# Optimization experiments

Measured on AMD Instinct MI355X. Metric: run time of the kernel, lower is better.

Reference implementation:

```python
import jax, jax.numpy as jnp
import numpy as np

N_NODES = 100000
N_EDGES = 500000
IN_FEATS = 128
HID = 128
OUT = 1


def setup_inputs() -> dict:
    key = jax.random.key(0)
    ks = jax.random.split(key, 10)
    h = jax.random.normal(ks[0], (N_NODES, IN_FEATS), dtype=jnp.float32)
    src = jax.random.randint(ks[1], (N_EDGES,), 0, N_NODES, dtype=jnp.int32)
    dst = jax.random.randint(ks[2], (N_EDGES,), 0, N_NODES, dtype=jnp.int32)
    # Linear params (PyTorch convention: W [out,in], y = x @ W.T + b)
    s1 = 1.0 / np.sqrt(2 * IN_FEATS)
    s2 = 1.0 / np.sqrt(HID)
    W1 = jax.random.uniform(ks[3], (HID, 2 * IN_FEATS), jnp.float32, -s1, s1)
    b1 = jax.random.uniform(ks[4], (HID,), jnp.float32, -s1, s1)
    W2 = jax.random.uniform(ks[5], (HID, HID), jnp.float32, -s2, s2)
    b2 = jax.random.uniform(ks[6], (HID,), jnp.float32, -s2, s2)
    W3 = jax.random.uniform(ks[7], (OUT, HID), jnp.float32, -s2, s2)
    b3 = jax.random.uniform(ks[8], (OUT,), jnp.float32, -s2, s2)
    return {"h": h, "src": src, "dst": dst,
            "W1": W1, "b1": b1, "W2": W2, "b2": b2, "W3": W3, "b3": b3}


def reference(h, src, dst, W1, b1, W2, b2, W3, b3):
    # Per-edge gather of src/dst node features. Instead of materializing the
    # [E, 2*in] concat, split W1 into its src/dst halves and fuse the concat
    # into two GEMMs (same math as fc1(cat([h_u, h_v], 1))).
    h_u = h[src]                                   # [E, in]
    h_v = h[dst]                                   # [E, in]
    W1u, W1v = W1[:, :IN_FEATS], W1[:, IN_FEATS:]  # [hid, in] each
    x = h_u @ W1u.T + h_v @ W1v.T + b1             # [E, hid]
    x = jax.nn.relu(x)
    x = jax.nn.relu(x @ W2.T + b2)                 # [E, hid]
    score = x @ W3.T + b3                          # [E, out]
    return score
```

## Files before the change

kernel.cpp:

```cpp
#include <hip/hip_runtime.h>
#include <hip/hip_bf16.h>
#include <hip/hip_fp16.h>


#define N_NODES 100000
#define N_EDGES 500000
#define F       128
#define HID     128
#define TE      64
#define NT      ((N_EDGES + TE - 1) / TE)
#define GRID    512
#define BLOCK   512

typedef _Float16 f16x8 __attribute__((ext_vector_type(8)));
typedef float    f32x4 __attribute__((ext_vector_type(4)));

typedef __attribute__((address_space(3))) unsigned int  lds_u32;
typedef __attribute__((address_space(1))) const unsigned int glb_u32;

__device__ __forceinline__ void load_lds16(const void* g, void* l) {
    __builtin_amdgcn_global_load_lds((glb_u32*)g, (lds_u32*)l, 16, 0, 0);
}

__device__ __forceinline__ void bar_lgkm() {
    asm volatile("s_waitcnt lgkmcnt(0)" ::: "memory");
    __builtin_amdgcn_s_barrier();
    __builtin_amdgcn_sched_barrier(0);
}
__device__ __forceinline__ void bar_vm() {
    asm volatile("s_waitcnt vmcnt(0) lgkmcnt(0)" ::: "memory");
    __builtin_amdgcn_s_barrier();
    __builtin_amdgcn_sched_barrier(0);
}

__global__ __launch_bounds__(256) void h_to_f16(const float* __restrict__ h,
                                                _Float16* __restrict__ h16) {
    const int i = (blockIdx.x * 256 + threadIdx.x) * 8;
    float4 a = *(const float4*)(h + i);
    float4 b = *(const float4*)(h + i + 4);
    f16x8 v;
    v[0] = (_Float16)a.x; v[1] = (_Float16)a.y; v[2] = (_Float16)a.z; v[3] = (_Float16)a.w;
    v[4] = (_Float16)b.x; v[5] = (_Float16)b.y; v[6] = (_Float16)b.z; v[7] = (_Float16)b.w;
    *(f16x8*)(h16 + i) = v;
}

__global__ __launch_bounds__(BLOCK) void edge_mlp_v2(
    const _Float16* __restrict__ h16,
    const int*   __restrict__ src,
    const int*   __restrict__ dst,
    const float* __restrict__ W1,
    const float* __restrict__ b1,
    const float* __restrict__ W2,
    const float* __restrict__ b2,
    const float* __restrict__ W3,
    const float* __restrict__ b3,
    float*       __restrict__ out)
{
    __shared__ __align__(128) char Alds[2 * TE * 512];
    __shared__ __align__(128) char Xlds[TE * 256];

    const int tid  = threadIdx.x;
    const int wave = tid >> 6;
    const int lane = tid & 63;
    const int l15  = lane & 15;
    const int lk   = lane >> 4;

    const int n1 = wave * 16 + l15;

    f16x8 w1f[8];
    #pragma unroll
    for (int kt = 0; kt < 8; ++kt) {
        const float* p = W1 + n1 * 256 + kt * 32 + lk * 8;
        f16x8 v;
        #pragma unroll
        for (int j = 0; j < 8; ++j) v[j] = (_Float16)p[j];
        w1f[kt] = v;
    }
    const float b1v = b1[n1];

    f16x8 w2f[4];
    #pragma unroll
    for (int kt = 0; kt < 4; ++kt) {
        const float* p = W2 + n1 * 128 + kt * 32 + lk * 8;
        f16x8 v;
        #pragma unroll
        for (int j = 0; j < 8; ++j) v[j] = (_Float16)p[j];
        w2f[kt] = v;
    }
    const float b2v = b2[n1];

    float w3r[16];
    {
        const float* p = W3 + (tid & 7) * 16;
        #pragma unroll
        for (int i = 0; i < 16; ++i) w3r[i] = p[i];
    }
    const float b3v = b3[0];

    int eloc[4], k16v[4];
    #pragma unroll
    for (int j = 0; j < 4; ++j) {
        const int i = wave * 4 + j;
        eloc[j] = 2 * i + (lane >> 5);
        k16v[j] = (l15) ^ (eloc[j] & 7);
    }
    const int whichv = (lane >> 4) & 1;
    const int* idxp  = whichv ? dst : src;

    const int t0 = blockIdx.x;

    int nodeCur[4], nodeNext[4];

    #pragma unroll
    for (int j = 0; j < 4; ++j) {
        int eg = t0 * TE + eloc[j];
        if (eg >= N_EDGES) eg = N_EDGES - 1;
        nodeCur[j] = idxp[eg];
    }
    #pragma unroll
    for (int j = 0; j < 4; ++j) {
        const _Float16* g = h16 + (size_t)nodeCur[j] * F + k16v[j] * 8;
        load_lds16(g, Alds + (wave * 4 + j) * 1024);
    }
    {
        int tn = t0 + GRID; if (tn > NT - 1) tn = NT - 1;
        #pragma unroll
        for (int j = 0; j < 4; ++j) {
            int eg = tn * TE + eloc[j];
            if (eg >= N_EDGES) eg = N_EDGES - 1;
            nodeNext[j] = idxp[eg];
        }
    }

    int cur = 0;
    for (int t = t0; t < NT; t += GRID) {
        bar_vm();

        #pragma unroll
        for (int j = 0; j < 4; ++j) nodeCur[j] = nodeNext[j];
        {
            char* nb = Alds + (cur ^ 1) * (TE * 512);
            #pragma unroll
            for (int j = 0; j < 4; ++j) {
                const _Float16* g = h16 + (size_t)nodeCur[j] * F + k16v[j] * 8;
                load_lds16(g, nb + (wave * 4 + j) * 1024);
            }
        }
        {
            int tn2 = t + 2 * GRID; if (tn2 > NT - 1) tn2 = NT - 1;
            #pragma unroll
            for (int j = 0; j < 4; ++j) {
                int eg = tn2 * TE + eloc[j];
                if (eg >= N_EDGES) eg = N_EDGES - 1;
                nodeNext[j] = idxp[eg];
            }
        }

        const char* Ab = Alds + cur * (TE * 512);

        #pragma unroll
        for (int m = 0; m < 4; ++m) {
            f32x4 acc = {0.f, 0.f, 0.f, 0.f};
            #pragma unroll
            for (int kt = 0; kt < 8; ++kt) {
                const int edge = m * 16 + l15;
                int byte = edge * 512 + (kt * 32 + lk * 8) * 2;
                byte ^= (edge & 7) << 4;
                f16x8 a = *(const f16x8*)(Ab + byte);
                acc = __builtin_amdgcn_mfma_f32_16x16x32_f16(a, w1f[kt], acc, 0, 0, 0);
            }
            #pragma unroll
            for (int r = 0; r < 4; ++r) {
                float v = acc[r] + b1v;
                v = v > 0.f ? v : 0.f;
                const int edge = m * 16 + lk * 4 + r;
                int byte = edge * 256 + n1 * 2;
                byte ^= (edge & 7) << 4;
                *(_Float16*)(Xlds + byte) = (_Float16)v;
            }
        }
        bar_lgkm();

        f32x4 acc2[4];
        #pragma unroll
        for (int m = 0; m < 4; ++m) {
            f32x4 acc = {0.f, 0.f, 0.f, 0.f};
            #pragma unroll
            for (int kt = 0; kt < 4; ++kt) {
                const int edge = m * 16 + l15;
                int byte = edge * 256 + (kt * 32 + lk * 8) * 2;
                byte ^= (edge & 7) << 4;
                f16x8 a = *(const f16x8*)(Xlds + byte);
                acc = __builtin_amdgcn_mfma_f32_16x16x32_f16(a, w2f[kt], acc, 0, 0, 0);
            }
            acc2[m] = acc;
        }
        bar_lgkm();
        #pragma unroll
        for (int m = 0; m < 4; ++m) {
            #pragma unroll
            for (int r = 0; r < 4; ++r) {
                float v = acc2[m][r] + b2v;
                v = v > 0.f ? v : 0.f;
                const int edge = m * 16 + lk * 4 + r;
                int byte = edge * 256 + n1 * 2;
                byte ^= (edge & 7) << 4;
                *(_Float16*)(Xlds + byte) = (_Float16)v;
            }
        }
        bar_lgkm();

        {
            const int e_loc = tid >> 3;
            const int cgrp  = tid & 7;
            const int swz   = (e_loc & 7) << 4;
            const int base  = e_loc * 256 + cgrp * 32;
            f16x8 x0 = *(const f16x8*)(Xlds + (base ^ swz));
            f16x8 x1 = *(const f16x8*)(Xlds + ((base + 16) ^ swz));
            float p = 0.f;
            #pragma unroll
            for (int i = 0; i < 8; ++i) p += (float)x0[i] * w3r[i];
            #pragma unroll
            for (int i = 0; i < 8; ++i) p += (float)x1[i] * w3r[8 + i];
            p += __shfl_xor(p, 1);
            p += __shfl_xor(p, 2);
            p += __shfl_xor(p, 4);
            const int eg = t * TE + e_loc;
            if (cgrp == 0 && eg < N_EDGES) out[eg] = p + b3v;
        }
        cur ^= 1;
    }
}

__global__ __launch_bounds__(BLOCK) void edge_mlp_v1(
    const float* __restrict__ h,
    const int*   __restrict__ src,
    const int*   __restrict__ dst,
    const float* __restrict__ W1,
    const float* __restrict__ b1,
    const float* __restrict__ W2,
    const float* __restrict__ b2,
    const float* __restrict__ W3,
    const float* __restrict__ b3,
    float*       __restrict__ out)
{
    __shared__ __align__(128) char Alds[TE * 512];
    __shared__ __align__(128) char Xlds[TE * 256];

    const int tid  = threadIdx.x;
    const int wave = tid >> 6;
    const int lane = tid & 63;
    const int l15  = lane & 15;
    const int lk   = lane >> 4;

    const int n1 = wave * 16 + l15;

    f16x8 w1f[8];
    #pragma unroll
    for (int kt = 0; kt < 8; ++kt) {
        const float* p = W1 + n1 * 256 + kt * 32 + lk * 8;
        f16x8 v;
        #pragma unroll
        for (int j = 0; j < 8; ++j) v[j] = (_Float16)p[j];
        w1f[kt] = v;
    }
    const float b1v = b1[n1];

    f16x8 w2f[4];
    #pragma unroll
    for (int kt = 0; kt < 4; ++kt) {
        const float* p = W2 + n1 * 128 + kt * 32 + lk * 8;
        f16x8 v;
        #pragma unroll
        for (int j = 0; j < 8; ++j) v[j] = (_Float16)p[j];
        w2f[kt] = v;
    }
    const float b2v = b2[n1];

    float w3r[16];
    {
        const float* p = W3 + (tid & 7) * 16;
        #pragma unroll
        for (int i = 0; i < 16; ++i) w3r[i] = p[i];
    }
    const float b3v = b3[0];

    const int slot    = tid >> 2;
    const int part    = tid & 3;
    const int g_e     = slot >> 1;
    const int g_which = slot & 1;

    for (int t = blockIdx.x; t < NT; t += gridDim.x) {
        {
            int eg = t * TE + g_e;
            if (eg >= N_EDGES) eg = N_EDGES - 1;
            const int node = g_which ? dst[eg] : src[eg];
            const float* p = h + node * F + part * 32;
            const int kbase = g_which * 128 + part * 32;
            #pragma unroll
            for (int c = 0; c < 4; ++c) {
                float4 v0 = *(const float4*)(p + c * 8);
                float4 v1 = *(const float4*)(p + c * 8 + 4);
                f16x8 x;
                x[0] = (_Float16)v0.x; x[1] = (_Float16)v0.y;
                x[2] = (_Float16)v0.z; x[3] = (_Float16)v0.w;
                x[4] = (_Float16)v1.x; x[5] = (_Float16)v1.y;
                x[6] = (_Float16)v1.z; x[7] = (_Float16)v1.w;
                int byte = g_e * 512 + (kbase + c * 8) * 2;
                byte ^= (g_e & 7) << 4;
                *(f16x8*)(Alds + byte) = x;
            }
        }
        __syncthreads();

        #pragma unroll
        for (int m = 0; m < 4; ++m) {
            f32x4 acc = {0.f, 0.f, 0.f, 0.f};
            #pragma unroll
            for (int kt = 0; kt < 8; ++kt) {
                const int edge = m * 16 + l15;
                int byte = edge * 512 + (kt * 32 + lk * 8) * 2;
                byte ^= (edge & 7) << 4;
                f16x8 a = *(const f16x8*)(Alds + byte);
                acc = __builtin_amdgcn_mfma_f32_16x16x32_f16(a, w1f[kt], acc, 0, 0, 0);
            }
            #pragma unroll
            for (int r = 0; r < 4; ++r) {
                float v = acc[r] + b1v;
                v = v > 0.f ? v : 0.f;
                const int edge = m * 16 + lk * 4 + r;
                int byte = edge * 256 + n1 * 2;
                byte ^= (edge & 7) << 4;
                *(_Float16*)(Xlds + byte) = (_Float16)v;
            }
        }
        __syncthreads();

        f32x4 acc2[4];
        #pragma unroll
        for (int m = 0; m < 4; ++m) {
            f32x4 acc = {0.f, 0.f, 0.f, 0.f};
            #pragma unroll
            for (int kt = 0; kt < 4; ++kt) {
                const int edge = m * 16 + l15;
                int byte = edge * 256 + (kt * 32 + lk * 8) * 2;
                byte ^= (edge & 7) << 4;
                f16x8 a = *(const f16x8*)(Xlds + byte);
                acc = __builtin_amdgcn_mfma_f32_16x16x32_f16(a, w2f[kt], acc, 0, 0, 0);
            }
            acc2[m] = acc;
        }
        __syncthreads();
        #pragma unroll
        for (int m = 0; m < 4; ++m) {
            #pragma unroll
            for (int r = 0; r < 4; ++r) {
                float v = acc2[m][r] + b2v;
                v = v > 0.f ? v : 0.f;
                const int edge = m * 16 + lk * 4 + r;
                int byte = edge * 256 + n1 * 2;
                byte ^= (edge & 7) << 4;
                *(_Float16*)(Xlds + byte) = (_Float16)v;
            }
        }
        __syncthreads();

        {
            const int e_loc = tid >> 3;
            const int cgrp  = tid & 7;
            const int swz   = (e_loc & 7) << 4;
            const int base  = e_loc * 256 + cgrp * 32;
            f16x8 x0 = *(const f16x8*)(Xlds + (base ^ swz));
            f16x8 x1 = *(const f16x8*)(Xlds + ((base + 16) ^ swz));
            float p = 0.f;
            #pragma unroll
            for (int i = 0; i < 8; ++i) p += (float)x0[i] * w3r[i];
            #pragma unroll
            for (int i = 0; i < 8; ++i) p += (float)x1[i] * w3r[8 + i];
            p += __shfl_xor(p, 1);
            p += __shfl_xor(p, 2);
            p += __shfl_xor(p, 4);
            const int eg = t * TE + e_loc;
            if (cgrp == 0 && eg < N_EDGES) out[eg] = p + b3v;
        }
    }
}

extern "C" void kernel_launch(void* const* d_in, const int* in_sizes, int n_in,
                              void* d_out, int out_size, void* d_ws, size_t ws_size,
                              hipStream_t stream) {
    const float* h   = (const float*)d_in[0];
    const int*   src = (const int*)  d_in[1];
    const int*   dst = (const int*)  d_in[2];
    const float* W1  = (const float*)d_in[3];
    const float* b1  = (const float*)d_in[4];
    const float* W2  = (const float*)d_in[5];
    const float* b2  = (const float*)d_in[6];
    const float* W3  = (const float*)d_in[7];
    const float* b3  = (const float*)d_in[8];
    float* out = (float*)d_out;

    const size_t need = (size_t)N_NODES * F * sizeof(_Float16);
    if (ws_size >= need) {
        _Float16* h16 = (_Float16*)d_ws;
        h_to_f16<<<6250, 256, 0, stream>>>(h, h16);
        edge_mlp_v2<<<GRID, BLOCK, 0, stream>>>(h16, src, dst, W1, b1, W2, b2, W3, b3, out);
    } else {
        edge_mlp_v1<<<GRID, BLOCK, 0, stream>>>(h, src, dst, W1, b1, W2, b2, W3, b3, out);
    }
}
```

Measured before the change: 211.8 us.

## Switch edge MLP to 32x32x16 MFMA with fused layer-3 epilogue

Replaces the 16x16x32 MFMA tiling with 32x32x16 MFMA, where each wave owns a 32-hidden by 32-edge tile with the weights as the A operand and the gathered features as B. The layer-2 output is reduced against W3 directly in registers and combined across waves through a small LDS partial-sum array. This removes one barrier and the LDS write and read round trip of the second hidden activation. It also widens the LDS swizzle to 16 rows, halves the grid to 256 blocks, and adds a launch-bounds occupancy hint, at the cost of more weight registers per thread.

```diff
diff --git a/kernel.cpp b/kernel.cpp
--- a/kernel.cpp
+++ b/kernel.cpp
@@ -9,11 +9,11 @@
 #define HID     128
 #define TE      64
 #define NT      ((N_EDGES + TE - 1) / TE)
-#define GRID    512
+#define GRID    256
 #define BLOCK   512
 
-typedef _Float16 f16x8 __attribute__((ext_vector_type(8)));
-typedef float    f32x4 __attribute__((ext_vector_type(4)));
+typedef _Float16 f16x8  __attribute__((ext_vector_type(8)));
+typedef float    f32x16 __attribute__((ext_vector_type(16)));
 
 typedef __attribute__((address_space(3))) unsigned int  lds_u32;
 typedef __attribute__((address_space(1))) const unsigned int glb_u32;
@@ -21,7 +21,6 @@
 __device__ __forceinline__ void load_lds16(const void* g, void* l) {
     __builtin_amdgcn_global_load_lds((glb_u32*)g, (lds_u32*)l, 16, 0, 0);
 }
-
 __device__ __forceinline__ void bar_lgkm() {
     asm volatile("s_waitcnt lgkmcnt(0)" ::: "memory");
     __builtin_amdgcn_s_barrier();
@@ -44,7 +43,7 @@
     *(f16x8*)(h16 + i) = v;
 }
 
-__global__ __launch_bounds__(BLOCK) void edge_mlp_v2(
+__global__ __launch_bounds__(BLOCK, 2) void edge_mlp_v3(
     const _Float16* __restrict__ h16,
     const int*   __restrict__ src,
     const int*   __restrict__ dst,
@@ -58,42 +57,41 @@
 {
     __shared__ __align__(128) char Alds[2 * TE * 512];
     __shared__ __align__(128) char Xlds[TE * 256];
+    __shared__ float Spart[8][32];
 
     const int tid  = threadIdx.x;
     const int wave = tid >> 6;
     const int lane = tid & 63;
-    const int l15  = lane & 15;
-    const int lk   = lane >> 4;
-
-    const int n1 = wave * 16 + l15;
-
-    f16x8 w1f[8];
+    const int mh   = wave >> 1;
+    const int ne   = wave & 1;
+    const int col  = lane & 31;
+    const int h    = lane >> 5;
+
+    f16x8 w1a[16];
+    #pragma unroll
+    for (int kt = 0; kt < 16; ++kt) {
+        const float* p = W1 + (mh * 32 + col) * 256 + kt * 16 + 8 * h;
+        f16x8 v;
+        #pragma unroll
+        for (int j = 0; j < 8; ++j) v[j] = (_Float16)p[j];
+        w1a[kt] = v;
+    }
+    f16x8 w2a[8];
     #pragma unroll
     for (int kt = 0; kt < 8; ++kt) {
-        const float* p = W1 + n1 * 256 + kt * 32 + lk * 8;
+        const float* p = W2 + (mh * 32 + col) * 128 + kt * 16 + 8 * h;
         f16x8 v;
         #pragma unroll
         for (int j = 0; j < 8; ++j) v[j] = (_Float16)p[j];
-        w1f[kt] = v;
-    }
-    const float b1v = b1[n1];
-
-    f16x8 w2f[4];
-    #pragma unroll
-    for (int kt = 0; kt < 4; ++kt) {
-        const float* p = W2 + n1 * 128 + kt * 32 + lk * 8;
-        f16x8 v;
-        #pragma unroll
-        for (int j = 0; j < 8; ++j) v[j] = (_Float16)p[j];
-        w2f[kt] = v;
-    }
-    const float b2v = b2[n1];
-
-    float w3r[16];
-    {
-        const float* p = W3 + (tid & 7) * 16;
-        #pragma unroll
-        for (int i = 0; i < 16; ++i) w3r[i] = p[i];
+        w2a[kt] = v;
+    }
+    float b1pl[16], b2pl[16], w3pl[16];
+    #pragma unroll
+    for (int r = 0; r < 16; ++r) {
+        const int row = mh * 32 + (r & 3) + 8 * (r >> 2) + 4 * h;
+        b1pl[r] = b1[row];
+        b2pl[r] = b2[row];
+        w3pl[r] = W3[row];
     }
     const float b3v = b3[0];
 
@@ -101,14 +99,13 @@
     #pragma unroll
     for (int j = 0; j < 4; ++j) {
         const int i = wave * 4 + j;
-        eloc[j] = 2 * i + (lane >> 5);
-        k16v[j] = (l15) ^ (eloc[j] & 7);
+        eloc[j] = 2 * i + h;
+        k16v[j] = (lane & 15) ^ (eloc[j] & 15);
     }
     const int whichv = (lane >> 4) & 1;
     const int* idxp  = whichv ? dst : src;
 
     const int t0 = blockIdx.x;
-
     int nodeCur[4], nodeNext[4];
 
     #pragma unroll
@@ -132,6 +129,9 @@
         }
     }
 
+    const int e_own = ne * 32 + col;
+    const int exor  = (e_own & 15) << 4;
+
     int cur = 0;
     for (int t = t0; t < NT; t += GRID) {
         bar_vm();
@@ -158,81 +158,58 @@
 
         const char* Ab = Alds + cur * (TE * 512);
 
-        #pragma unroll
-        for (int m = 0; m < 4; ++m) {
-            f32x4 acc = {0.f, 0.f, 0.f, 0.f};
-            #pragma unroll
-            for (int kt = 0; kt < 8; ++kt) {
-                const int edge = m * 16 + l15;
-                int byte = edge * 512 + (kt * 32 + lk * 8) * 2;
-                byte ^= (edge & 7) << 4;
-                f16x8 a = *(const f16x8*)(Ab + byte);
-                acc = __builtin_amdgcn_mfma_f32_16x16x32_f16(a, w1f[kt], acc, 0, 0, 0);
-            }
-            #pragma unroll
-            for (int r = 0; r < 4; ++r) {
-                float v = acc[r] + b1v;
-                v = v > 0.f ? v : 0.f;
-                const int edge = m * 16 + lk * 4 + r;
-                int byte = edge * 256 + n1 * 2;
-                byte ^= (edge & 7) << 4;
-                *(_Float16*)(Xlds + byte) = (_Float16)v;
-            }
+        f32x16 acc1 = {};
+        #pragma unroll
+        for (int kt = 0; kt < 16; ++kt) {
+            const int c = (kt * 32 + 16 * h) ^ exor;
+            f16x8 bf = *(const f16x8*)(Ab + e_own * 512 + c);
+            acc1 = __builtin_amdgcn_mfma_f32_32x32x16_f16(w1a[kt], bf, acc1, 0, 0, 0);
+        }
+        #pragma unroll
+        for (int pr = 0; pr < 8; ++pr) {
+            float v0 = acc1[2 * pr]     + b1pl[2 * pr];
+            float v1 = acc1[2 * pr + 1] + b1pl[2 * pr + 1];
+            v0 = v0 > 0.f ? v0 : 0.f;
+            v1 = v1 > 0.f ? v1 : 0.f;
+            union { _Float16 q[2]; unsigned u; } pk;
+            pk.q[0] = (_Float16)v0; pk.q[1] = (_Float16)v1;
+            const int row0 = mh * 32 + ((2 * pr) & 3) + 8 * (pr >> 1) + 4 * h;
+            const int c = (row0 * 2) ^ exor;
+            *(unsigned*)(Xlds + e_own * 256 + c) = pk.u;
         }
         bar_lgkm();
 
-        f32x4 acc2[4];
-        #pragma unroll
-        for (int m = 0; m < 4; ++m) {
-            f32x4 acc = {0.f, 0.f, 0.f, 0.f};
-            #pragma unroll
-            for (int kt = 0; kt < 4; ++kt) {
-                const int edge = m * 16 + l15;
-                int byte = edge * 256 + (kt * 32 + lk * 8) * 2;
-                byte ^= (edge & 7) << 4;
-                f16x8 a = *(const f16x8*)(Xlds + byte);
-                acc = __builtin_amdgcn_mfma_f32_16x16x32_f16(a, w2f[kt], acc, 0, 0, 0);
-            }
-            acc2[m] = acc;
-        }
+        f32x16 acc2 = {};
+        #pragma unroll
+        for (int kt = 0; kt < 8; ++kt) {
+            const int c = (kt * 32 + 16 * h) ^ exor;
+            f16x8 xf = *(const f16x8*)(Xlds + e_own * 256 + c);
+            acc2 = __builtin_amdgcn_mfma_f32_32x32x16_f16(w2a[kt], xf, acc2, 0, 0, 0);
+        }
+
+        float p = 0.f;
+        #pragma unroll
+        for (int r = 0; r < 16; ++r) {
+            float v = acc2[r] + b2pl[r];
+            v = v > 0.f ? v : 0.f;
+            p = fmaf(w3pl[r], v, p);
+        }
+        p += __shfl_xor(p, 32);
+        if (lane < 32) Spart[wave][lane] = p;
         bar_lgkm();
-        #pragma unroll
-        for (int m = 0; m < 4; ++m) {
-            #pragma unroll
-            for (int r = 0; r < 4; ++r) {
-                float v = acc2[m][r] + b2v;
-                v = v > 0.f ? v : 0.f;
-                const int edge = m * 16 + lk * 4 + r;
-                int byte = edge * 256 + n1 * 2;
-                byte ^= (edge & 7) << 4;
-                *(_Float16*)(Xlds + byte) = (_Float16)v;
-            }
-        }
-        bar_lgkm();
-
-        {
-            const int e_loc = tid >> 3;
-            const int cgrp  = tid & 7;
-            const int swz   = (e_loc & 7) << 4;
-            const int base  = e_loc * 256 + cgrp * 32;
-            f16x8 x0 = *(const f16x8*)(Xlds + (base ^ swz));
-            f16x8 x1 = *(const f16x8*)(Xlds + ((base + 16) ^ swz));
-            float p = 0.f;
-            #pragma unroll
-            for (int i = 0; i < 8; ++i) p += (float)x0[i] * w3r[i];
-            #pragma unroll
-            for (int i = 0; i < 8; ++i) p += (float)x1[i] * w3r[8 + i];
-            p += __shfl_xor(p, 1);
-            p += __shfl_xor(p, 2);
-            p += __shfl_xor(p, 4);
-            const int eg = t * TE + e_loc;
-            if (cgrp == 0 && eg < N_EDGES) out[eg] = p + b3v;
+
+        if (tid < TE) {
+            const int eg = t * TE + tid;
+            const int w0 = tid >> 5, c0 = tid & 31;
+            float s = Spart[w0][c0] + Spart[2 + w0][c0]
+                    + Spart[4 + w0][c0] + Spart[6 + w0][c0] + b3v;
+            if (eg < N_EDGES) out[eg] = s;
         }
         cur ^= 1;
     }
 }
 
-__global__ __launch_bounds__(BLOCK) void edge_mlp_v1(
+__global__ __launch_bounds__(512) void edge_mlp_v1(
     const float* __restrict__ h,
     const int*   __restrict__ src,
     const int*   __restrict__ dst,
@@ -246,13 +223,13 @@
 {
     __shared__ __align__(128) char Alds[TE * 512];
     __shared__ __align__(128) char Xlds[TE * 256];
+    typedef float f32x4 __attribute__((ext_vector_type(4)));
 
     const int tid  = threadIdx.x;
     const int wave = tid >> 6;
     const int lane = tid & 63;
     const int l15  = lane & 15;
     const int lk   = lane >> 4;
-
     const int n1 = wave * 16 + l15;
 
     f16x8 w1f[8];
@@ -265,7 +242,6 @@
         w1f[kt] = v;
     }
     const float b1v = b1[n1];
-
     f16x8 w2f[4];
     #pragma unroll
     for (int kt = 0; kt < 4; ++kt) {
@@ -276,7 +252,6 @@
         w2f[kt] = v;
     }
     const float b2v = b2[n1];
-
     float w3r[16];
     {
         const float* p = W3 + (tid & 7) * 16;
@@ -285,10 +260,8 @@
     }
     const float b3v = b3[0];
 
-    const int slot    = tid >> 2;
-    const int part    = tid & 3;
-    const int g_e     = slot >> 1;
-    const int g_which = slot & 1;
+    const int slot = tid >> 2, part = tid & 3;
+    const int g_e = slot >> 1, g_which = slot & 1;
 
     for (int t = blockIdx.x; t < NT; t += gridDim.x) {
         {
@@ -312,7 +285,6 @@
             }
         }
         __syncthreads();
-
         #pragma unroll
         for (int m = 0; m < 4; ++m) {
             f32x4 acc = {0.f, 0.f, 0.f, 0.f};
@@ -335,7 +307,6 @@
             }
         }
         __syncthreads();
-
         f32x4 acc2[4];
         #pragma unroll
         for (int m = 0; m < 4; ++m) {
@@ -364,7 +335,6 @@
             }
         }
         __syncthreads();
-
         {
             const int e_loc = tid >> 3;
             const int cgrp  = tid & 7;
@@ -404,8 +374,8 @@
     if (ws_size >= need) {
         _Float16* h16 = (_Float16*)d_ws;
         h_to_f16<<<6250, 256, 0, stream>>>(h, h16);
-        edge_mlp_v2<<<GRID, BLOCK, 0, stream>>>(h16, src, dst, W1, b1, W2, b2, W3, b3, out);
+        edge_mlp_v3<<<GRID, BLOCK, 0, stream>>>(h16, src, dst, W1, b1, W2, b2, W3, b3, out);
     } else {
-        edge_mlp_v1<<<GRID, BLOCK, 0, stream>>>(h, src, dst, W1, b1, W2, b2, W3, b3, out);
-    }
-}
+        edge_mlp_v1<<<512, 512, 0, stream>>>(h, src, dst, W1, b1, W2, b2, W3, b3, out);
+    }
+}
```

Result: faster. 184.6 us (-12.8%).
